# Kernel optimization log

Measured on AMD Instinct MI355X. Metric: run time of the kernel, lower is better.

## Reference

```python
import jax, jax.numpy as jnp
import numpy as np
jax.config.update("jax_enable_x64", True)
from jax.scipy.special import i0e

P = 256            # feature_num / contrast_dim
C = 1000           # num_classes
N = 512            # batch
TEMPERATURE = 1.0
ORDER = P // 2 - 1 # Bessel order nu = p/2 - 1


def _normalize(x, axis=-1, eps=1e-12):
    n = jnp.linalg.norm(x, axis=axis, keepdims=True)
    return x / jnp.maximum(n, eps)


def miller_recurrence(order, kappa):
    """Vectorized Miller backward recurrence for log I_order(k), log I_{order+1}(k).
    kappa: float64 array of any shape. Returns (log_I_order_scaled, log_I_order1_scaled)
    matching the torch reference (exponentially-scaled via i0e)."""
    ones = jnp.ones(kappa.shape, jnp.float64)
    zeros = jnp.zeros(kappa.shape, jnp.float64)
    init = (ones, zeros, zeros, zeros, zeros, zeros, zeros)
    iis = jnp.arange(2 * order, 0, -1)

    def step(carry, i):
        I_n, I_n1, scale, scale0, scale1, E0, E1 = carry
        coef = (2.0 * i) / kappa
        I_t = coef * I_n + I_n1
        ovf = jnp.any(jnp.isinf(I_t))  # global rescale trigger, as in torch
        logI = jnp.log(I_n)
        I_n1_r = I_n1 / I_n
        I_n_r = coef + I_n1_r          # recompute with I_n reset to 1
        I_n_new = jnp.where(ovf, I_n_r, I_t)
        I_n1_new = jnp.where(ovf, jnp.ones_like(I_n), I_n)
        scale = jnp.where(ovf, scale + logI, scale)
        scale0 = jnp.where(ovf & (i >= order), scale0 + logI, scale0)
        scale1 = jnp.where(ovf & (i >= order + 1), scale1 + logI, scale1)
        E0 = jnp.where(i == order, I_n1_new, E0)
        E1 = jnp.where(i == order + 1, I_n1_new, E1)
        return (I_n_new, I_n1_new, scale, scale0, scale1, E0, E1), None

    (I_n, _, scale, scale0, scale1, E0, E1), _ = jax.lax.scan(step, init, iis)
    live0 = jnp.log(i0e(kappa))
    e0 = live0 + jnp.log(E0) - jnp.log(I_n) + scale0 - scale
    e1 = live0 + jnp.log(E1) - jnp.log(I_n) + scale1 - scale
    return e0, e1


def setup_inputs() -> dict:
    key = jax.random.key(0)
    k1, k2, k3, k4 = jax.random.split(key, 4)
    features = jax.random.normal(k1, (N, P), dtype=jnp.float32)
    labels = jax.random.randint(k2, (N,), 0, C)
    real_span_mask = jax.random.randint(k3, (N,), 0, 2).astype(bool)
    Ave = (_normalize(jax.random.normal(k4, (C, P), dtype=jnp.float32), axis=1) * 0.9).astype(jnp.float32)
    Amount = jnp.zeros((C,), jnp.float32)
    return {"features": features, "labels": labels, "real_span_mask": real_span_mask,
            "Ave": Ave, "Amount": Amount}


def reference(features, labels, real_span_mask, Ave, Amount):
    feats = jax.lax.stop_gradient(features)
    # --- update_CV (masked rows contribute nothing, equivalent to boolean select) ---
    m = real_span_mask.astype(feats.dtype)                       # (N,)
    onehot = jax.nn.one_hot(labels, C, dtype=feats.dtype) * m[:, None]  # (N,C)
    counts = onehot.sum(0)                                       # (C,)
    feat_sum = jnp.einsum('nc,na->ca', onehot, feats)            # (C,A)
    denom = jnp.where(counts == 0, 1.0, counts)
    ave_CxA = feat_sum / denom[:, None]
    w = counts / (counts + Amount)
    w = jnp.where(jnp.isnan(w), 0.0, w)
    Ave_new = Ave * (1.0 - w[:, None]) + ave_CxA * w[:, None]    # (C,A)
    # --- update_kappa ---
    R = jnp.linalg.norm(Ave_new, axis=1)
    kappa = P * R / (1.0 - R ** 2)
    kappa = jnp.where((kappa > 1e5) | (kappa < 0), 1e5, kappa)   # f32 (C,)
    nu, _ = miller_recurrence(ORDER, kappa.astype(jnp.float64))
    logc = nu + kappa - (P / 2 - 1) * jnp.log(kappa + 1e-20)     # f64 (C,)
    # --- logits ---
    Ave_norm = _normalize(Ave_new, axis=1)
    temp = kappa[:, None] * Ave_norm                             # (C,A) f32
    t = temp[None, :, :] + features[:, None, :] / TEMPERATURE    # (N,C,A)
    kappa_new = jnp.linalg.norm(t, axis=2)                       # (N,C) f32
    nu_k, _ = miller_recurrence(ORDER, kappa_new.astype(jnp.float64))
    logits = (nu_k + kappa_new - (P / 2 - 1) * jnp.log(kappa_new + 1e-20)
              - logc[None, :]).astype(jnp.float32)
    return _normalize(logits, axis=1)
```

## Files before the change

kernel.cpp:

```cpp
#include <hip/hip_runtime.h>

static constexpr int NN = 512, CC = 1000, PP = 256, ORD = 127;

static constexpr size_t OFF_TEMPT  = 0;
static constexpr size_t OFF_LOGC   = 1024000;
static constexpr size_t OFF_T2     = 1032000;
static constexpr size_t OFF_F2     = 1040000;
static constexpr size_t OFF_LOGITS = 1048576;

__global__ __launch_bounds__(256) void k_prep(
    const float* __restrict__ feats, const unsigned* __restrict__ A,
    const unsigned* __restrict__ B, const float* __restrict__ Ave,
    const float* __restrict__ Amount, float* __restrict__ tempT,
    double* __restrict__ logcv, double* __restrict__ T2,
    double* __restrict__ F2)
{
    __shared__ float  red4[4];
    __shared__ double redd[4];
    __shared__ int    s_list[64];
    __shared__ int    s_lcnt, s_fl0, s_fl1;
    const int c = blockIdx.x, tid = threadIdx.x;

    if (tid == 0) { s_lcnt = 0; s_fl0 = 0; s_fl1 = 0; }
    __syncthreads();
    int f0 = 0, f1 = 0;
    for (int w = tid; w < NN; w += 256) {
        if (A[w] > 1u) f0 = 1;
        if (B[w] > 1u) f1 = 1;
    }
    if (f0) atomicOr(&s_fl0, 1);
    if (f1) atomicOr(&s_fl1, 1);
    __syncthreads();
    const bool a_is_lab = s_fl0 ? true : (s_fl1 ? false : true);
    const unsigned* LAB = a_is_lab ? A : B;
    const unsigned* MSK = a_is_lab ? B : A;

    if (c < NN) {
        float v = feats[c * PP + tid];
        double ss = (double)v * (double)v;
        for (int off = 32; off > 0; off >>= 1) ss += __shfl_down(ss, off);
        if ((tid & 63) == 0) redd[tid >> 6] = ss;
        __syncthreads();
        if (tid == 0) F2[c] = redd[0] + redd[1] + redd[2] + redd[3];
        __syncthreads();
    }

    for (int n = tid; n < NN; n += 256) {
        if (MSK[n] != 0u && (int)LAB[n] == c) {
            int i = atomicAdd(&s_lcnt, 1);
            if (i < 64) s_list[i] = n;
        }
    }
    __syncthreads();
    const int lc = s_lcnt < 64 ? s_lcnt : 64;
    float sum = 0.f;
    for (int i = 0; i < lc; ++i) sum += feats[s_list[i] * PP + tid];

    float cntf   = (float)s_lcnt;
    float amount = Amount[c];
    float w = cntf / (cntf + amount);
    if (isnan(w)) w = 0.f;
    float denom = (cntf == 0.f) ? 1.f : cntf;
    float ave = sum / denom;
    float av_new = Ave[c * PP + tid] * (1.f - w) + ave * w;

    float ss2 = av_new * av_new;
    for (int off = 32; off > 0; off >>= 1) ss2 += __shfl_down(ss2, off);
    if ((tid & 63) == 0) red4[tid >> 6] = ss2;
    __syncthreads();
    float tot = red4[0] + red4[1] + red4[2] + red4[3];

    float R = sqrtf(tot);
    float kf = 256.0f * R / (1.0f - R * R);
    if (kf > 1e5f || kf < 0.0f) kf = 1e5f;
    float mu = av_new / fmaxf(R, 1e-12f);
    float tv = kf * mu;
    tempT[tid * CC + c] = tv;

    double ts = (double)tv * (double)tv;
    for (int off = 32; off > 0; off >>= 1) ts += __shfl_down(ts, off);
    if ((tid & 63) == 0) redd[tid >> 6] = ts;
    __syncthreads();

    if (tid == 0) {
        T2[c] = redd[0] + redd[1] + redd[2] + redd[3];
        float invf = 1.0f / kf;
        float In = 1.f, In1 = 0.f, i2 = 508.f;
        for (int it = 0; it < ORD; ++it) {
            float t = fmaf(i2 * invf, In, In1); In1 = In; In = t; i2 -= 2.f;
        }
        float E0 = In;
        for (int it = 0; it < ORD; ++it) {
            float t = fmaf(i2 * invf, In, In1); In1 = In; In = t; i2 -= 2.f;
        }
        float x = 0.125f * invf;
        float pser = x * (1.f + x * (4.5f + x * (37.5f + x * 459.375f)));
        float l1p = pser - 0.5f * pser * pser;
        float lr = logf(E0 / In);
        float lk = logf(kf);
        logcv[c] = (double)(l1p + lr) - 0.9189385332046727
                   + (double)kf - 127.5 * (double)lk;
    }
}

__global__ __launch_bounds__(256) void k_main(
    const float* __restrict__ feats, const float* __restrict__ tempT,
    const double* __restrict__ T2, const double* __restrict__ F2,
    const double* __restrict__ logcv, float* __restrict__ logits)
{
    __shared__ float f_s[2][PP];
    const int tid = threadIdx.x;
    const int n0  = blockIdx.y * 2;
    const int c   = blockIdx.x * 256 + tid;
    #pragma unroll
    for (int j = 0; j < 2; ++j)
        f_s[j][tid] = feats[(n0 + j) * PP + tid];
    __syncthreads();
    const bool act = (c < CC);

    float a0 = 0.f, a1 = 0.f;
    if (act) {
        #pragma unroll 8
        for (int a = 0; a < PP; ++a) {
            float tv = tempT[a * CC + c];
            a0 = fmaf(tv, f_s[0][a], a0);
            a1 = fmaf(tv, f_s[1][a], a1);
        }
    }
    float accs[2] = {a0, a1};
    double t2c = act ? T2[c] : 1.0e6;
    double kd[2];
    float kf[2], invf[2], In[2], In1[2], E0[2];
    #pragma unroll
    for (int j = 0; j < 2; ++j) {
        double kk = act ? (t2c + 2.0 * (double)accs[j] + F2[n0 + j]) : 1.0e6;
        kd[j]  = (double)(float)sqrt(kk);
        kf[j]  = (float)kd[j];
        invf[j] = 1.0f / kf[j];
        In[j] = 1.f; In1[j] = 0.f;
    }
    float i2 = 508.f;
    for (int it = 0; it < ORD; ++it) {
        #pragma unroll
        for (int j = 0; j < 2; ++j) {
            float t = fmaf(i2 * invf[j], In[j], In1[j]);
            In1[j] = In[j]; In[j] = t;
        }
        i2 -= 2.f;
    }
    #pragma unroll
    for (int j = 0; j < 2; ++j) E0[j] = In[j];
    for (int it = 0; it < ORD; ++it) {
        #pragma unroll
        for (int j = 0; j < 2; ++j) {
            float t = fmaf(i2 * invf[j], In[j], In1[j]);
            In1[j] = In[j]; In[j] = t;
        }
        i2 -= 2.f;
    }
    if (!act) return;
    double lgc = logcv[c];
    #pragma unroll
    for (int j = 0; j < 2; ++j) {
        float x = 0.125f * invf[j];
        float pser = x * (1.f + x * (4.5f + x * (37.5f + x * 459.375f)));
        float l1p = pser - 0.5f * pser * pser;
        float lr = logf(E0[j] / In[j]);
        float lk = logf(kf[j]);
        double lg = (double)(l1p + lr) - 0.9189385332046727
                    + kd[j] - 127.5 * (double)lk - lgc;
        logits[(n0 + j) * CC + c] = (float)lg;
    }
}

__global__ __launch_bounds__(256) void k_norm(
    const float* __restrict__ logits, float* __restrict__ out)
{
    __shared__ double red4[4];
    const int n = blockIdx.x;
    const int tid = threadIdx.x;
    float v[4];
    double ss = 0.0;
    #pragma unroll
    for (int q = 0; q < 4; ++q) {
        int c = tid + q * 256;
        v[q] = (c < CC) ? logits[n * CC + c] : 0.f;
        ss += (double)v[q] * (double)v[q];
    }
    for (int off = 32; off > 0; off >>= 1) ss += __shfl_down(ss, off);
    if ((tid & 63) == 0) red4[tid >> 6] = ss;
    __syncthreads();
    double tot = red4[0] + red4[1] + red4[2] + red4[3];
    float inv = 1.0f / fmaxf((float)sqrt(tot), 1e-12f);
    #pragma unroll
    for (int q = 0; q < 4; ++q) {
        int c = tid + q * 256;
        if (c < CC) out[n * CC + c] = v[q] * inv;
    }
}

extern "C" void kernel_launch(void* const* d_in, const int* in_sizes, int n_in,
                              void* d_out, int out_size, void* d_ws, size_t ws_size,
                              hipStream_t stream) {
    int i_feat = -1, i_ave = -1, i_amt = -1, i5a = -1, i5b = -1;
    for (int i = 0; i < n_in; ++i) {
        int s = in_sizes[i];
        if      (s == NN * PP) i_feat = i;
        else if (s == CC * PP) i_ave  = i;
        else if (s == CC)      i_amt  = i;
        else if (s == NN)      { if (i5a < 0) i5a = i; else i5b = i; }
    }
    if (i_feat < 0 || i_ave < 0 || i_amt < 0 || i5a < 0 || i5b < 0) {
        i_feat = 0; i5a = 1; i5b = 2; i_ave = 3; i_amt = 4;
    }
    const float*    feats  = (const float*)d_in[i_feat];
    const unsigned* bufA   = (const unsigned*)d_in[i5a];
    const unsigned* bufB   = (const unsigned*)d_in[i5b];
    const float*    Ave    = (const float*)d_in[i_ave];
    const float*    Amount = (const float*)d_in[i_amt];

    char* ws = (char*)d_ws;
    float*  tempT  = (float*)(ws + OFF_TEMPT);
    double* logcv  = (double*)(ws + OFF_LOGC);
    double* T2     = (double*)(ws + OFF_T2);
    double* F2     = (double*)(ws + OFF_F2);
    float*  logits = (float*)(ws + OFF_LOGITS);
    float*  out    = (float*)d_out;

    k_prep<<<dim3(CC), dim3(256), 0, stream>>>(feats, bufA, bufB, Ave, Amount,
                                               tempT, logcv, T2, F2);
    k_main<<<dim3(4, NN / 2), dim3(256), 0, stream>>>(feats, tempT, T2, F2,
                                                      logcv, logits);
    k_norm<<<dim3(NN), dim3(256), 0, stream>>>(logits, out);
}
```

Baseline: 97.11 us.

## Split main kernel into 8-row GEMM and separate Bessel-recurrence kernel

The fused dot-product plus Miller recurrence kernel is split in two. A dedicated GEMM kernel computes eight feature rows per block, so each tempT load is reused across eight rows instead of two, and writes the dot products to a workspace buffer. A second kernel reads those values and runs the serial recurrence. This cuts redundant tempT traffic and separates the memory-bound phase from the latency-bound ALU phase, at the cost of an extra launch and a 2 MB intermediate write and read.

```diff
diff --git a/kernel.cpp b/kernel.cpp
--- a/kernel.cpp
+++ b/kernel.cpp
@@ -7,6 +7,7 @@
 static constexpr size_t OFF_T2     = 1032000;
 static constexpr size_t OFF_F2     = 1040000;
 static constexpr size_t OFF_LOGITS = 1048576;
+static constexpr size_t OFF_D      = 3145728;
 
 __global__ __launch_bounds__(256) void k_prep(
     const float* __restrict__ feats, const unsigned* __restrict__ A,
@@ -103,32 +104,51 @@
     }
 }
 
-__global__ __launch_bounds__(256) void k_main(
+__global__ __launch_bounds__(256) void k_gemm(
     const float* __restrict__ feats, const float* __restrict__ tempT,
-    const double* __restrict__ T2, const double* __restrict__ F2,
-    const double* __restrict__ logcv, float* __restrict__ logits)
-{
-    __shared__ float f_s[2][PP];
+    float* __restrict__ D)
+{
+    __shared__ float f_s[8][PP];
+    const int tid = threadIdx.x;
+    const int n0  = blockIdx.y * 8;
+    const int c   = blockIdx.x * 256 + tid;
+    #pragma unroll
+    for (int j = 0; j < 8; ++j)
+        f_s[j][tid] = feats[(n0 + j) * PP + tid];
+    __syncthreads();
+    if (c >= CC) return;
+
+    float acc[8] = {0.f, 0.f, 0.f, 0.f, 0.f, 0.f, 0.f, 0.f};
+    #pragma unroll 8
+    for (int a = 0; a < PP; ++a) {
+        float tv = tempT[a * CC + c];
+        #pragma unroll
+        for (int j = 0; j < 8; ++j)
+            acc[j] = fmaf(tv, f_s[j][a], acc[j]);
+    }
+    #pragma unroll
+    for (int j = 0; j < 8; ++j)
+        D[(n0 + j) * CC + c] = acc[j];
+}
+
+__global__ __launch_bounds__(256) void k_chain(
+    const float* __restrict__ D, const double* __restrict__ T2,
+    const double* __restrict__ F2, const double* __restrict__ logcv,
+    float* __restrict__ logits)
+{
     const int tid = threadIdx.x;
     const int n0  = blockIdx.y * 2;
     const int c   = blockIdx.x * 256 + tid;
-    #pragma unroll
-    for (int j = 0; j < 2; ++j)
-        f_s[j][tid] = feats[(n0 + j) * PP + tid];
-    __syncthreads();
     const bool act = (c < CC);
 
-    float a0 = 0.f, a1 = 0.f;
+    float d0 = 0.f, d1 = 0.f;
+    double t2c = 1.0e6;
     if (act) {
-        #pragma unroll 8
-        for (int a = 0; a < PP; ++a) {
-            float tv = tempT[a * CC + c];
-            a0 = fmaf(tv, f_s[0][a], a0);
-            a1 = fmaf(tv, f_s[1][a], a1);
-        }
-    }
-    float accs[2] = {a0, a1};
-    double t2c = act ? T2[c] : 1.0e6;
+        d0 = D[n0 * CC + c];
+        d1 = D[(n0 + 1) * CC + c];
+        t2c = T2[c];
+    }
+    float accs[2] = {d0, d1};
     double kd[2];
     float kf[2], invf[2], In[2], In1[2], E0[2];
     #pragma unroll
@@ -225,11 +245,12 @@
     double* T2     = (double*)(ws + OFF_T2);
     double* F2     = (double*)(ws + OFF_F2);
     float*  logits = (float*)(ws + OFF_LOGITS);
+    float*  Dm     = (float*)(ws + OFF_D);
     float*  out    = (float*)d_out;
 
     k_prep<<<dim3(CC), dim3(256), 0, stream>>>(feats, bufA, bufB, Ave, Amount,
                                                tempT, logcv, T2, F2);
-    k_main<<<dim3(4, NN / 2), dim3(256), 0, stream>>>(feats, tempT, T2, F2,
-                                                      logcv, logits);
+    k_gemm<<<dim3(4, NN / 8), dim3(256), 0, stream>>>(feats, tempT, Dm);
+    k_chain<<<dim3(4, NN / 2), dim3(256), 0, stream>>>(Dm, T2, F2, logcv, logits);
     k_norm<<<dim3(NN), dim3(256), 0, stream>>>(logits, out);
 }
```

Result: slower. 154.4 us (+59.0%).
